# Optimization experiments

Measured on AMD Instinct MI355X. Metric: run time of the kernel, lower is better.

Reference implementation:

```python
import jax, jax.numpy as jnp
import numpy as np

GROUPS = 32
EPS = 1e-6


def setup_inputs() -> dict:
    key = jax.random.key(0)
    ks = jax.random.split(key, 8)
    B, H, W, D, C = 4, 16, 16, 16, 512
    s = 1.0 / np.sqrt(C)  # lecun-normal-ish scale for dense kernels
    return {
        "x": jax.random.normal(ks[0], (B, H, W, D, C), dtype=jnp.float32),
        "gn_scale": jnp.ones((C,), jnp.float32),
        "gn_bias": jnp.zeros((C,), jnp.float32),
        "wq": jax.random.normal(ks[1], (C, C), jnp.float32) * s,
        "bq": jnp.zeros((C,), jnp.float32),
        "wk": jax.random.normal(ks[2], (C, C), jnp.float32) * s,
        "bk": jnp.zeros((C,), jnp.float32),
        "wv": jax.random.normal(ks[3], (C, C), jnp.float32) * s,
        "bv": jnp.zeros((C,), jnp.float32),
        "wp": jax.random.normal(ks[4], (C, C), jnp.float32) * s,
        "bp": jnp.zeros((C,), jnp.float32),
    }


def _group_norm(x, scale, bias):
    B, H, W, D, C = x.shape
    xg = x.reshape(B, H, W, D, GROUPS, C // GROUPS)
    mean = xg.mean(axis=(1, 2, 3, 5), keepdims=True)
    var = xg.var(axis=(1, 2, 3, 5), keepdims=True)
    xn = (xg - mean) * jax.lax.rsqrt(var + EPS)
    return xn.reshape(B, H, W, D, C) * scale + bias


def reference(x, gn_scale, gn_bias, wq, bq, wk, bk, wv, bv, wp, bp):
    B, H, W, D, C = x.shape
    h = _group_norm(x, gn_scale, gn_bias)
    hf = h.reshape(B, H * W * D, C)  # flatten spatial (attention axes 1,2,3)
    q = hf @ wq + bq
    k = hf @ wk + bk
    v = hf @ wv + bv
    # full dot-product attention over flattened (H,W,D) tokens, single head
    q = q * (C ** -0.5)
    logits = jnp.einsum("bqc,bkc->bqk", q, k)  # [B, N, N]
    attn = jax.nn.softmax(logits, axis=-1)
    o = jnp.einsum("bqk,bkc->bqc", attn, v)
    o = o @ wp + bp
    return x + o.reshape(B, H, W, D, C)
```

## Files before the change

### kernel.cpp

```cpp
#include <hip/hip_runtime.h>
#include <stdint.h>

typedef __bf16  bf16x8 __attribute__((ext_vector_type(8)));
typedef short   s16x8  __attribute__((ext_vector_type(8)));
typedef float   f32x4  __attribute__((ext_vector_type(4)));

__device__ inline short f2bf(float f) {
  union { float f; uint32_t u; } v; v.f = f;
  uint32_t r = v.u + 0x7FFFu + ((v.u >> 16) & 1u);
  return (short)(r >> 16);
}


__global__ __launch_bounds__(256) void gn_stats_k(const float* __restrict__ x,
                                                  float* __restrict__ mean,
                                                  float* __restrict__ rstd) {
  int bg = blockIdx.x;
  int b = bg >> 5, g = bg & 31;
  int tid = threadIdx.x;
  const float* base = x + (size_t)b * 4096 * 512 + g * 16;
  float s = 0.f, q = 0.f;
  for (int i = tid; i < 16384; i += 256) {
    int n = i >> 2, sub = i & 3;
    float4 v = *(const float4*)(base + (size_t)n * 512 + sub * 4);
    s += v.x + v.y + v.z + v.w;
    q += v.x * v.x + v.y * v.y + v.z * v.z + v.w * v.w;
  }
  for (int off = 32; off > 0; off >>= 1) {
    s += __shfl_down(s, off, 64);
    q += __shfl_down(q, off, 64);
  }
  __shared__ float rs[4], rq[4];
  int w = tid >> 6;
  if ((tid & 63) == 0) { rs[w] = s; rq[w] = q; }
  __syncthreads();
  if (tid == 0) {
    float S = rs[0] + rs[1] + rs[2] + rs[3];
    float Q = rq[0] + rq[1] + rq[2] + rq[3];
    float m = S * (1.f / 65536.f);
    float var = Q * (1.f / 65536.f) - m * m;
    mean[bg] = m;
    rstd[bg] = rsqrtf(var + 1e-6f);
  }
}

__global__ __launch_bounds__(256) void gn_apply_k(const float* __restrict__ x,
                                                  const float* __restrict__ mean,
                                                  const float* __restrict__ rstd,
                                                  const float* __restrict__ sc,
                                                  const float* __restrict__ bi,
                                                  short* __restrict__ h) {
  size_t i4 = ((size_t)blockIdx.x * 256 + threadIdx.x) * 4;
  int c = (int)(i4 & 511);
  int tok = (int)(i4 >> 9);
  int b = tok >> 12;
  int bg = b * 32 + (c >> 4);
  float m = mean[bg], r = rstd[bg];
  float4 v = *(const float4*)(x + i4);
  float4 s = *(const float4*)(sc + c);
  float4 bb = *(const float4*)(bi + c);
  short4 o;
  o.x = f2bf((v.x - m) * r * s.x + bb.x);
  o.y = f2bf((v.y - m) * r * s.y + bb.y);
  o.z = f2bf((v.z - m) * r * s.z + bb.z);
  o.w = f2bf((v.w - m) * r * s.w + bb.w);
  *(short4*)(h + i4) = o;
}

__global__ __launch_bounds__(256) void wconv_k(const float* __restrict__ wq,
                                               const float* __restrict__ wk,
                                               const float* __restrict__ wv,
                                               const float* __restrict__ wp,
                                               short* __restrict__ wt) {
  int i = blockIdx.x * 256 + threadIdx.x;
  int widx = i >> 18, rem = i & 262143;
  int c = rem >> 9, j = rem & 511;
  const float* w = widx == 0 ? wq : widx == 1 ? wk : widx == 2 ? wv : wp;
  wt[(size_t)widx * 262144 + (size_t)j * 512 + c] = f2bf(w[(size_t)c * 512 + j]);
}

__global__ __launch_bounds__(256) void gemm_k(const short* __restrict__ A,
                                              const short* __restrict__ Bt,
                                              const float* __restrict__ bias,
                                              const float* __restrict__ xres,
                                              short* __restrict__ outb,
                                              float* __restrict__ outf, int mode) {
  __shared__ __attribute__((aligned(16))) short As[128 * 32];
  __shared__ __attribute__((aligned(16))) short Bs[128 * 32];
  int tid = threadIdx.x;
  int w = tid >> 6, lane = tid & 63, quad = lane >> 4, mrow = lane & 15;
  int wm = w >> 1, wn = w & 1;
  int m0 = blockIdx.x * 128, n0 = blockIdx.y * 128;

  const f32x4 fz = {0.f, 0.f, 0.f, 0.f};
  f32x4 acc[4][4];
#pragma unroll
  for (int i = 0; i < 4; i++)
#pragma unroll
    for (int j = 0; j < 4; j++) acc[i][j] = fz;

  int srow = tid >> 2;
  int scol = (tid & 3) * 8;

  for (int k0 = 0; k0 < 512; k0 += 32) {
    __syncthreads();
#pragma unroll
    for (int i = 0; i < 2; i++) {
      const short* ga = A + (size_t)(m0 + i * 64 + srow) * 512 + k0 + scol;
      const short* gb = Bt + (size_t)(n0 + i * 64 + srow) * 512 + k0 + scol;
      char* la = (char*)As + i * 4096 + w * 1024;
      char* lb = (char*)Bs + i * 4096 + w * 1024;
      __builtin_amdgcn_global_load_lds((__attribute__((address_space(1))) void*)ga,
                                       (__attribute__((address_space(3))) void*)la, 16, 0, 0);
      __builtin_amdgcn_global_load_lds((__attribute__((address_space(1))) void*)gb,
                                       (__attribute__((address_space(3))) void*)lb, 16, 0, 0);
    }
    __syncthreads();
    bf16x8 af[4], bfv[4];
#pragma unroll
    for (int mi = 0; mi < 4; mi++)
      af[mi] = *(const bf16x8*)&As[(wm * 64 + mi * 16 + mrow) * 32 + quad * 8];
#pragma unroll
    for (int ni = 0; ni < 4; ni++)
      bfv[ni] = *(const bf16x8*)&Bs[(wn * 64 + ni * 16 + mrow) * 32 + quad * 8];
#pragma unroll
    for (int mi = 0; mi < 4; mi++)
#pragma unroll
      for (int ni = 0; ni < 4; ni++)
        acc[mi][ni] = __builtin_amdgcn_mfma_f32_16x16x32_bf16(af[mi], bfv[ni], acc[mi][ni], 0, 0, 0);
  }

#pragma unroll
  for (int mi = 0; mi < 4; mi++)
#pragma unroll
    for (int ni = 0; ni < 4; ni++) {
      int col = n0 + wn * 64 + ni * 16 + mrow;
      float bv = bias[col];
#pragma unroll
      for (int r = 0; r < 4; r++) {
        int row = m0 + wm * 64 + mi * 16 + quad * 4 + r;
        float val = acc[mi][ni][r] + bv;
        if (mode == 0) {
          outb[(size_t)row * 512 + col] = f2bf(val);
        } else if (mode == 1) {
          int b = row >> 12, t = row & 4095;
          outb[(size_t)b * (512 * 4096) + (size_t)col * 4096 + t] = f2bf(val);
        } else {
          size_t idx = (size_t)row * 512 + col;
          outf[idx] = xres[idx] + val;
        }
      }
    }
}

__global__ __launch_bounds__(256, 1) void flash_k(const short* __restrict__ Q,
                                                  const short* __restrict__ K,
                                                  const short* __restrict__ Vt,
                                                  short* __restrict__ O) {
  __shared__ __attribute__((aligned(16))) short Ks[2][16384];
  int L = blockIdx.x;
  int b = (L & 7) >> 1;
  int q0 = (((L >> 3) << 1) | (L & 1)) * 64;
  int tid = threadIdx.x;
  int w = tid >> 6, lane = tid & 63, quad = lane >> 4, m = lane & 15;
  const size_t batch_off = (size_t)b * 4096 * 512;
  const float scale2 = 0.06375872f;

  bf16x8 qf[16];
#pragma unroll
  for (int s = 0; s < 16; s++)
    qf[s] = *(const bf16x8*)&Q[batch_off + (size_t)(q0 + w * 16 + m) * 512 + s * 32 + quad * 8];

  const f32x4 fz = {0.f, 0.f, 0.f, 0.f};
  f32x4 oacc[32];
#pragma unroll
  for (int i = 0; i < 32; i++) oacc[i] = fz;
  float mrun = -1e30f, lrun = 0.f;

#pragma unroll
  for (int i = 0; i < 8; i++) {
    int ksb = w * 16 + i * 2;
    const short* gk = K + batch_off + (size_t)(lane & 31) * 512 + (size_t)(ksb + (lane >> 5)) * 8;
    __builtin_amdgcn_global_load_lds((__attribute__((address_space(1))) void*)gk,
                                     (__attribute__((address_space(3))) void*)&Ks[0][ksb * 256],
                                     16, 0, 0);
  }

  for (int it = 0; it < 128; ++it) {
    int t0 = it * 32;
    int buf = it & 1;
    __syncthreads();
    if (it < 127) {
      int t1 = t0 + 32;
#pragma unroll
      for (int i = 0; i < 8; i++) {
        int ksb = w * 16 + i * 2;
        const short* gk = K + batch_off + (size_t)(t1 + (lane & 31)) * 512 +
                          (size_t)(ksb + (lane >> 5)) * 8;
        __builtin_amdgcn_global_load_lds((__attribute__((address_space(1))) void*)gk,
                                         (__attribute__((address_space(3))) void*)&Ks[buf ^ 1][ksb * 256],
                                         16, 0, 0);
      }
    }
    bf16x8 vf[32];
#pragma unroll
    for (int ct = 0; ct < 32; ct++)
      vf[ct] = *(const bf16x8*)&Vt[batch_off + (size_t)(ct * 16 + m) * 4096 + t0 + quad * 8];
    f32x4 s0a = fz, s0b = fz, s1a = fz, s1b = fz;
#pragma unroll
    for (int s = 0; s < 16; s++) {
      bf16x8 k0 = *(const bf16x8*)&Ks[buf][((s * 4 + quad) * 32 + m) * 8];
      bf16x8 k1 = *(const bf16x8*)&Ks[buf][((s * 4 + quad) * 32 + 16 + m) * 8];
      if (s & 1) {
        s0b = __builtin_amdgcn_mfma_f32_16x16x32_bf16(k0, qf[s], s0b, 0, 0, 0);
        s1b = __builtin_amdgcn_mfma_f32_16x16x32_bf16(k1, qf[s], s1b, 0, 0, 0);
      } else {
        s0a = __builtin_amdgcn_mfma_f32_16x16x32_bf16(k0, qf[s], s0a, 0, 0, 0);
        s1a = __builtin_amdgcn_mfma_f32_16x16x32_bf16(k1, qf[s], s1a, 0, 0, 0);
      }
    }
    float v0[4], v1[4];
    float mx = -1e30f;
#pragma unroll
    for (int r = 0; r < 4; r++) {
      v0[r] = (s0a[r] + s0b[r]) * scale2;
      v1[r] = (s1a[r] + s1b[r]) * scale2;
      mx = fmaxf(mx, fmaxf(v0[r], v1[r]));
    }
    mx = fmaxf(mx, __shfl_xor(mx, 16, 64));
    mx = fmaxf(mx, __shfl_xor(mx, 32, 64));
    float mn = fmaxf(mrun, mx);
    float alpha = exp2f(mrun - mn);
    mrun = mn;
    float p0[4], p1[4];
    float sum = 0.f;
#pragma unroll
    for (int r = 0; r < 4; r++) {
      p0[r] = exp2f(v0[r] - mn);
      p1[r] = exp2f(v1[r] - mn);
      sum += p0[r] + p1[r];
    }
    sum += __shfl_xor(sum, 16, 64);
    sum += __shfl_xor(sum, 32, 64);
    lrun = lrun * alpha + sum;
    if (__any(alpha != 1.0f)) {
      float al[4];
#pragma unroll
      for (int r = 0; r < 4; r++) al[r] = __shfl(alpha, quad * 4 + r, 64);
#pragma unroll
      for (int i = 0; i < 32; i++)
#pragma unroll
        for (int r = 0; r < 4; r++) oacc[i][r] *= al[r];
    }
    s16x8 pfs;
#pragma unroll
    for (int j = 0; j < 8; j++) {
      int src = ((((quad & 1) * 2 + (j >> 2)) << 4) | m);
      float a0 = __shfl(p0[j & 3], src, 64);
      float a1 = __shfl(p1[j & 3], src, 64);
      pfs[j] = f2bf(quad < 2 ? a0 : a1);
    }
    bf16x8 pf = __builtin_bit_cast(bf16x8, pfs);
#pragma unroll
    for (int ct = 0; ct < 32; ct++)
      oacc[ct] = __builtin_amdgcn_mfma_f32_16x16x32_bf16(pf, vf[ct], oacc[ct], 0, 0, 0);
  }
  float invl = 1.f / lrun;
  float inv[4];
#pragma unroll
  for (int r = 0; r < 4; r++) inv[r] = __shfl(invl, quad * 4 + r, 64);
#pragma unroll
  for (int ct = 0; ct < 32; ct++)
#pragma unroll
    for (int r = 0; r < 4; r++) {
      int row = q0 + w * 16 + quad * 4 + r;
      int col = ct * 16 + m;
      O[batch_off + (size_t)row * 512 + col] = f2bf(oacc[ct][r] * inv[r]);
    }
}

extern "C" void kernel_launch(void* const* d_in, const int* in_sizes, int n_in,
                              void* d_out, int out_size, void* d_ws, size_t ws_size,
                              hipStream_t stream) {
  const float* x  = (const float*)d_in[0];
  const float* gs = (const float*)d_in[1];
  const float* gb = (const float*)d_in[2];
  const float* wq = (const float*)d_in[3];
  const float* bq = (const float*)d_in[4];
  const float* wk = (const float*)d_in[5];
  const float* bk = (const float*)d_in[6];
  const float* wv = (const float*)d_in[7];
  const float* bv = (const float*)d_in[8];
  const float* wp = (const float*)d_in[9];
  const float* bp = (const float*)d_in[10];
  float* out = (float*)d_out;

  char* ws = (char*)d_ws;
  float* mean = (float*)ws;
  float* rstd = (float*)(ws + 512);
  short* h    = (short*)(ws + 1024);
  short* wt   = (short*)(ws + 1024 + 16777216);
  short* Vt   = (short*)(ws + 1024 + 16777216 + 2097152);
  short* Qb   = (short*)d_out;
  short* Kb   = Qb + 8388608;
  short* Ob   = h;

  gn_stats_k<<<128, 256, 0, stream>>>(x, mean, rstd);
  gn_apply_k<<<8192, 256, 0, stream>>>(x, mean, rstd, gs, gb, h);
  wconv_k<<<4096, 256, 0, stream>>>(wq, wk, wv, wp, wt);
  dim3 gg(128, 4);
  gemm_k<<<gg, 256, 0, stream>>>(h, wt,          bq, nullptr, Qb, nullptr, 0);
  gemm_k<<<gg, 256, 0, stream>>>(h, wt + 262144, bk, nullptr, Kb, nullptr, 0);
  gemm_k<<<gg, 256, 0, stream>>>(h, wt + 524288, bv, nullptr, Vt, nullptr, 1);
  flash_k<<<256, 256, 0, stream>>>(Qb, Kb, Vt, Ob);
  gemm_k<<<gg, 256, 0, stream>>>(Ob, wt + 786432, bp, x, nullptr, out, 2);
}
```

Measured before the change: 848.6 us.

## Split flash attention keys across waves and drop LDS K staging

Each block now handles 32 query rows instead of 64, and its four waves split as two query tiles by two halves of the key sequence. The two halves are merged at the end through shared memory using a split-softmax combine. The grid doubles to 512 blocks, with launch bounds raised to allow two blocks per CU. K is now read directly from global memory instead of through double-buffered LDS, and V is loaded per MFMA rather than prefetched into registers. The aim is more parallelism and occupancy, at the cost of less K reuse within a block, more global and cache traffic, and an extra merge step.

```diff
diff --git a/kernel.cpp b/kernel.cpp
--- a/kernel.cpp
+++ b/kernel.cpp
@@ -153,23 +153,26 @@
     }
 }
 
-__global__ __launch_bounds__(256, 1) void flash_k(const short* __restrict__ Q,
+__global__ __launch_bounds__(256, 2) void flash_k(const short* __restrict__ Q,
                                                   const short* __restrict__ K,
                                                   const short* __restrict__ Vt,
                                                   short* __restrict__ O) {
-  __shared__ __attribute__((aligned(16))) short Ks[2][16384];
+  __shared__ float Oz[2][16][512];
+  __shared__ float mS[2][2][16], lS[2][2][16];
   int L = blockIdx.x;
   int b = (L & 7) >> 1;
-  int q0 = (((L >> 3) << 1) | (L & 1)) * 64;
+  int q0 = (((L >> 3) << 1) | (L & 1)) * 32;
   int tid = threadIdx.x;
   int w = tid >> 6, lane = tid & 63, quad = lane >> 4, m = lane & 15;
+  int qt = w & 1, kc = w >> 1;
   const size_t batch_off = (size_t)b * 4096 * 512;
   const float scale2 = 0.06375872f;
 
+  const short* Qrow = Q + batch_off + (size_t)(q0 + qt * 16 + m) * 512;
   bf16x8 qf[16];
 #pragma unroll
   for (int s = 0; s < 16; s++)
-    qf[s] = *(const bf16x8*)&Q[batch_off + (size_t)(q0 + w * 16 + m) * 512 + s * 32 + quad * 8];
+    qf[s] = *(const bf16x8*)&Qrow[s * 32 + quad * 8];
 
   const f32x4 fz = {0.f, 0.f, 0.f, 0.f};
   f32x4 oacc[32];
@@ -177,40 +180,17 @@
   for (int i = 0; i < 32; i++) oacc[i] = fz;
   float mrun = -1e30f, lrun = 0.f;
 
-#pragma unroll
-  for (int i = 0; i < 8; i++) {
-    int ksb = w * 16 + i * 2;
-    const short* gk = K + batch_off + (size_t)(lane & 31) * 512 + (size_t)(ksb + (lane >> 5)) * 8;
-    __builtin_amdgcn_global_load_lds((__attribute__((address_space(1))) void*)gk,
-                                     (__attribute__((address_space(3))) void*)&Ks[0][ksb * 256],
-                                     16, 0, 0);
-  }
-
-  for (int it = 0; it < 128; ++it) {
-    int t0 = it * 32;
-    int buf = it & 1;
-    __syncthreads();
-    if (it < 127) {
-      int t1 = t0 + 32;
-#pragma unroll
-      for (int i = 0; i < 8; i++) {
-        int ksb = w * 16 + i * 2;
-        const short* gk = K + batch_off + (size_t)(t1 + (lane & 31)) * 512 +
-                          (size_t)(ksb + (lane >> 5)) * 8;
-        __builtin_amdgcn_global_load_lds((__attribute__((address_space(1))) void*)gk,
-                                         (__attribute__((address_space(3))) void*)&Ks[buf ^ 1][ksb * 256],
-                                         16, 0, 0);
-      }
-    }
-    bf16x8 vf[32];
-#pragma unroll
-    for (int ct = 0; ct < 32; ct++)
-      vf[ct] = *(const bf16x8*)&Vt[batch_off + (size_t)(ct * 16 + m) * 4096 + t0 + quad * 8];
+  const int tbase = kc * 2048;
+#pragma unroll 1
+  for (int it = 0; it < 64; ++it) {
+    int t0 = tbase + it * 32;
     f32x4 s0a = fz, s0b = fz, s1a = fz, s1b = fz;
+    const short* Kr0 = K + batch_off + (size_t)(t0 + m) * 512;
+    const short* Kr1 = K + batch_off + (size_t)(t0 + 16 + m) * 512;
 #pragma unroll
     for (int s = 0; s < 16; s++) {
-      bf16x8 k0 = *(const bf16x8*)&Ks[buf][((s * 4 + quad) * 32 + m) * 8];
-      bf16x8 k1 = *(const bf16x8*)&Ks[buf][((s * 4 + quad) * 32 + 16 + m) * 8];
+      bf16x8 k0 = *(const bf16x8*)&Kr0[s * 32 + quad * 8];
+      bf16x8 k1 = *(const bf16x8*)&Kr1[s * 32 + quad * 8];
       if (s & 1) {
         s0b = __builtin_amdgcn_mfma_f32_16x16x32_bf16(k0, qf[s], s0b, 0, 0, 0);
         s1b = __builtin_amdgcn_mfma_f32_16x16x32_bf16(k1, qf[s], s1b, 0, 0, 0);
@@ -261,22 +241,46 @@
       pfs[j] = f2bf(quad < 2 ? a0 : a1);
     }
     bf16x8 pf = __builtin_bit_cast(bf16x8, pfs);
+    const short* Vr = Vt + batch_off + (size_t)m * 4096 + t0 + quad * 8;
+#pragma unroll
+    for (int ct = 0; ct < 32; ct++) {
+      bf16x8 vf = *(const bf16x8*)&Vr[(size_t)ct * 16 * 4096];
+      oacc[ct] = __builtin_amdgcn_mfma_f32_16x16x32_bf16(pf, vf, oacc[ct], 0, 0, 0);
+    }
+  }
+  if (lane < 16) { mS[qt][kc][lane] = mrun; lS[qt][kc][lane] = lrun; }
+  __syncthreads();
+  float mo = mS[qt][kc ^ 1][m];
+  float mt = fmaxf(mrun, mo);
+  float f  = exp2f(mrun - mt);
+  float fr[4];
+#pragma unroll
+  for (int r = 0; r < 4; r++) fr[r] = __shfl(f, quad * 4 + r, 64);
+  if (kc == 1) {
 #pragma unroll
     for (int ct = 0; ct < 32; ct++)
-      oacc[ct] = __builtin_amdgcn_mfma_f32_16x16x32_bf16(pf, vf[ct], oacc[ct], 0, 0, 0);
-  }
-  float invl = 1.f / lrun;
-  float inv[4];
-#pragma unroll
-  for (int r = 0; r < 4; r++) inv[r] = __shfl(invl, quad * 4 + r, 64);
-#pragma unroll
-  for (int ct = 0; ct < 32; ct++)
-#pragma unroll
-    for (int r = 0; r < 4; r++) {
-      int row = q0 + w * 16 + quad * 4 + r;
-      int col = ct * 16 + m;
-      O[batch_off + (size_t)row * 512 + col] = f2bf(oacc[ct][r] * inv[r]);
-    }
+#pragma unroll
+      for (int r = 0; r < 4; r++)
+        Oz[qt][quad * 4 + r][ct * 16 + m] = oacc[ct][r] * fr[r];
+  }
+  __syncthreads();
+  if (kc == 0) {
+    float m1 = mS[qt][1][m], l1 = lS[qt][1][m];
+    float ltot = lrun * f + l1 * exp2f(m1 - mt);
+    float invl = 1.f / ltot;
+    float ir[4];
+#pragma unroll
+    for (int r = 0; r < 4; r++) ir[r] = __shfl(invl, quad * 4 + r, 64);
+#pragma unroll
+    for (int ct = 0; ct < 32; ct++)
+#pragma unroll
+      for (int r = 0; r < 4; r++) {
+        float val = oacc[ct][r] * fr[r] + Oz[qt][quad * 4 + r][ct * 16 + m];
+        int row = q0 + qt * 16 + quad * 4 + r;
+        int col = ct * 16 + m;
+        O[batch_off + (size_t)row * 512 + col] = f2bf(val * ir[r]);
+      }
+  }
 }
 
 extern "C" void kernel_launch(void* const* d_in, const int* in_sizes, int n_in,
@@ -312,6 +316,6 @@
   gemm_k<<<gg, 256, 0, stream>>>(h, wt,          bq, nullptr, Qb, nullptr, 0);
   gemm_k<<<gg, 256, 0, stream>>>(h, wt + 262144, bk, nullptr, Kb, nullptr, 0);
   gemm_k<<<gg, 256, 0, stream>>>(h, wt + 524288, bv, nullptr, Vt, nullptr, 1);
-  flash_k<<<256, 256, 0, stream>>>(Qb, Kb, Vt, Ob);
+  flash_k<<<512, 256, 0, stream>>>(Qb, Kb, Vt, Ob);
   gemm_k<<<gg, 256, 0, stream>>>(Ob, wt + 786432, bp, x, nullptr, out, 2);
 }
```

Result: slower. 1.135 ms (+33.8%).

## Split flash attention waves across output channels with smaller query tiles

Applied to the files above, without the earlier changes.

The flash kernel now gives each block 16 query rows instead of 64. Its four waves split the 512 output channels (128 each) rather than the query rows, and the grid grows from 256 to 1024 blocks with a two-blocks-per-CU launch bound. This cuts the output accumulator registers fourfold and prefetches the next V tile into registers one iteration ahead. The P fragments are also packed to bf16 before the shuffle, halving the shuffle count. In exchange, every wave recomputes the same QK^T scores, and K is streamed into LDS four times as often overall.

```diff
diff --git a/kernel.cpp b/kernel.cpp
--- a/kernel.cpp
+++ b/kernel.cpp
@@ -10,6 +10,7 @@
   uint32_t r = v.u + 0x7FFFu + ((v.u >> 16) & 1u);
   return (short)(r >> 16);
 }
+__device__ inline uint32_t f2bf_u(float f) { return (uint32_t)(uint16_t)f2bf(f); }
 
 
 __global__ __launch_bounds__(256) void gn_stats_k(const float* __restrict__ x,
@@ -153,28 +154,30 @@
     }
 }
 
-__global__ __launch_bounds__(256, 1) void flash_k(const short* __restrict__ Q,
+__global__ __launch_bounds__(256, 2) void flash_k(const short* __restrict__ Q,
                                                   const short* __restrict__ K,
                                                   const short* __restrict__ Vt,
                                                   short* __restrict__ O) {
   __shared__ __attribute__((aligned(16))) short Ks[2][16384];
   int L = blockIdx.x;
   int b = (L & 7) >> 1;
-  int q0 = (((L >> 3) << 1) | (L & 1)) * 64;
+  int qt = ((L >> 3) << 1) | (L & 1);
+  int q0 = qt * 16;
   int tid = threadIdx.x;
   int w = tid >> 6, lane = tid & 63, quad = lane >> 4, m = lane & 15;
   const size_t batch_off = (size_t)b * 4096 * 512;
   const float scale2 = 0.06375872f;
 
+  const short* Qrow = Q + batch_off + (size_t)(q0 + m) * 512;
   bf16x8 qf[16];
 #pragma unroll
   for (int s = 0; s < 16; s++)
-    qf[s] = *(const bf16x8*)&Q[batch_off + (size_t)(q0 + w * 16 + m) * 512 + s * 32 + quad * 8];
+    qf[s] = *(const bf16x8*)&Qrow[s * 32 + quad * 8];
 
   const f32x4 fz = {0.f, 0.f, 0.f, 0.f};
-  f32x4 oacc[32];
-#pragma unroll
-  for (int i = 0; i < 32; i++) oacc[i] = fz;
+  f32x4 oacc[8];
+#pragma unroll
+  for (int i = 0; i < 8; i++) oacc[i] = fz;
   float mrun = -1e30f, lrun = 0.f;
 
 #pragma unroll
@@ -186,6 +189,13 @@
                                      16, 0, 0);
   }
 
+  const short* Vbase = Vt + batch_off + (size_t)(w * 128 + m) * 4096 + quad * 8;
+  bf16x8 vc[8];
+#pragma unroll
+  for (int ct = 0; ct < 8; ct++)
+    vc[ct] = *(const bf16x8*)&Vbase[(size_t)ct * 16 * 4096];
+
+#pragma unroll 1
   for (int it = 0; it < 128; ++it) {
     int t0 = it * 32;
     int buf = it & 1;
@@ -202,10 +212,13 @@
                                          16, 0, 0);
       }
     }
-    bf16x8 vf[32];
-#pragma unroll
-    for (int ct = 0; ct < 32; ct++)
-      vf[ct] = *(const bf16x8*)&Vt[batch_off + (size_t)(ct * 16 + m) * 4096 + t0 + quad * 8];
+    bf16x8 vn[8];
+    if (it < 127) {
+      int t1 = t0 + 32;
+#pragma unroll
+      for (int ct = 0; ct < 8; ct++)
+        vn[ct] = *(const bf16x8*)&Vbase[(size_t)ct * 16 * 4096 + t1];
+    }
     f32x4 s0a = fz, s0b = fz, s1a = fz, s1b = fz;
 #pragma unroll
     for (int s = 0; s < 16; s++) {
@@ -248,34 +261,41 @@
 #pragma unroll
       for (int r = 0; r < 4; r++) al[r] = __shfl(alpha, quad * 4 + r, 64);
 #pragma unroll
-      for (int i = 0; i < 32; i++)
+      for (int i = 0; i < 8; i++)
 #pragma unroll
         for (int r = 0; r < 4; r++) oacc[i][r] *= al[r];
     }
+    uint32_t pk[4];
+#pragma unroll
+    for (int r = 0; r < 4; r++)
+      pk[r] = f2bf_u(p0[r]) | (f2bf_u(p1[r]) << 16);
     s16x8 pfs;
 #pragma unroll
     for (int j = 0; j < 8; j++) {
       int src = ((((quad & 1) * 2 + (j >> 2)) << 4) | m);
-      float a0 = __shfl(p0[j & 3], src, 64);
-      float a1 = __shfl(p1[j & 3], src, 64);
-      pfs[j] = f2bf(quad < 2 ? a0 : a1);
+      uint32_t pv = (uint32_t)__shfl((int)pk[j & 3], src, 64);
+      pfs[j] = (short)(quad < 2 ? (pv & 0xffffu) : (pv >> 16));
     }
     bf16x8 pf = __builtin_bit_cast(bf16x8, pfs);
 #pragma unroll
-    for (int ct = 0; ct < 32; ct++)
-      oacc[ct] = __builtin_amdgcn_mfma_f32_16x16x32_bf16(pf, vf[ct], oacc[ct], 0, 0, 0);
+    for (int ct = 0; ct < 8; ct++)
+      oacc[ct] = __builtin_amdgcn_mfma_f32_16x16x32_bf16(pf, vc[ct], oacc[ct], 0, 0, 0);
+    if (it < 127) {
+#pragma unroll
+      for (int ct = 0; ct < 8; ct++) vc[ct] = vn[ct];
+    }
   }
   float invl = 1.f / lrun;
-  float inv[4];
-#pragma unroll
-  for (int r = 0; r < 4; r++) inv[r] = __shfl(invl, quad * 4 + r, 64);
-#pragma unroll
-  for (int ct = 0; ct < 32; ct++)
+  float ir[4];
+#pragma unroll
+  for (int r = 0; r < 4; r++) ir[r] = __shfl(invl, quad * 4 + r, 64);
+#pragma unroll
+  for (int ct = 0; ct < 8; ct++)
 #pragma unroll
     for (int r = 0; r < 4; r++) {
-      int row = q0 + w * 16 + quad * 4 + r;
-      int col = ct * 16 + m;
-      O[batch_off + (size_t)row * 512 + col] = f2bf(oacc[ct][r] * inv[r]);
+      int row = q0 + quad * 4 + r;
+      int col = w * 128 + ct * 16 + m;
+      O[batch_off + (size_t)row * 512 + col] = f2bf(oacc[ct][r] * ir[r]);
     }
 }
 
@@ -312,6 +332,6 @@
   gemm_k<<<gg, 256, 0, stream>>>(h, wt,          bq, nullptr, Qb, nullptr, 0);
   gemm_k<<<gg, 256, 0, stream>>>(h, wt + 262144, bk, nullptr, Kb, nullptr, 0);
   gemm_k<<<gg, 256, 0, stream>>>(h, wt + 524288, bv, nullptr, Vt, nullptr, 1);
-  flash_k<<<256, 256, 0, stream>>>(Qb, Kb, Vt, Ob);
+  flash_k<<<1024, 256, 0, stream>>>(Qb, Kb, Vt, Ob);
   gemm_k<<<gg, 256, 0, stream>>>(Ob, wt + 786432, bp, x, nullptr, out, 2);
 }
```

Result: slower. 1.300 ms (+53.2%).

## Stage V tiles through double-buffered LDS and pack P bf16 before shuffling

Applied to the files above, without the earlier changes.

Each block now loads the V^T tile for the next key step into a second double-buffered LDS array with async global_load_lds, alongside K. Previously every wave read all 32 V fragments straight from global memory on each iteration. The P fragment is converted to bf16 and two values are packed per 32-bit register before the cross-lane shuffle, which halves the shuffle count. LDS use doubles to 128KB and the occupancy hint in launch_bounds is dropped, which may limit residency to one block per CU.

```diff
diff --git a/kernel.cpp b/kernel.cpp
--- a/kernel.cpp
+++ b/kernel.cpp
@@ -10,6 +10,7 @@
   uint32_t r = v.u + 0x7FFFu + ((v.u >> 16) & 1u);
   return (short)(r >> 16);
 }
+__device__ inline uint32_t f2bf_u(float f) { return (uint32_t)(uint16_t)f2bf(f); }
 
 
 __global__ __launch_bounds__(256) void gn_stats_k(const float* __restrict__ x,
@@ -153,11 +154,12 @@
     }
 }
 
-__global__ __launch_bounds__(256, 1) void flash_k(const short* __restrict__ Q,
-                                                  const short* __restrict__ K,
-                                                  const short* __restrict__ Vt,
-                                                  short* __restrict__ O) {
+__global__ __launch_bounds__(256) void flash_k(const short* __restrict__ Q,
+                                               const short* __restrict__ K,
+                                               const short* __restrict__ Vt,
+                                               short* __restrict__ O) {
   __shared__ __attribute__((aligned(16))) short Ks[2][16384];
+  __shared__ __attribute__((aligned(16))) short Vs[2][16384];
   int L = blockIdx.x;
   int b = (L & 7) >> 1;
   int q0 = (((L >> 3) << 1) | (L & 1)) * 64;
@@ -166,10 +168,11 @@
   const size_t batch_off = (size_t)b * 4096 * 512;
   const float scale2 = 0.06375872f;
 
+  const short* Qrow = Q + batch_off + (size_t)(q0 + w * 16 + m) * 512;
   bf16x8 qf[16];
 #pragma unroll
   for (int s = 0; s < 16; s++)
-    qf[s] = *(const bf16x8*)&Q[batch_off + (size_t)(q0 + w * 16 + m) * 512 + s * 32 + quad * 8];
+    qf[s] = *(const bf16x8*)&Qrow[s * 32 + quad * 8];
 
   const f32x4 fz = {0.f, 0.f, 0.f, 0.f};
   f32x4 oacc[32];
@@ -185,7 +188,16 @@
                                      (__attribute__((address_space(3))) void*)&Ks[0][ksb * 256],
                                      16, 0, 0);
   }
-
+#pragma unroll
+  for (int i = 0; i < 8; i++) {
+    int ct = w * 8 + i;
+    const short* gv = Vt + batch_off + (size_t)(ct * 16 + m) * 4096 + quad * 8;
+    __builtin_amdgcn_global_load_lds((__attribute__((address_space(1))) void*)gv,
+                                     (__attribute__((address_space(3))) void*)&Vs[0][ct * 512],
+                                     16, 0, 0);
+  }
+
+#pragma unroll 1
   for (int it = 0; it < 128; ++it) {
     int t0 = it * 32;
     int buf = it & 1;
@@ -201,11 +213,15 @@
                                          (__attribute__((address_space(3))) void*)&Ks[buf ^ 1][ksb * 256],
                                          16, 0, 0);
       }
-    }
-    bf16x8 vf[32];
-#pragma unroll
-    for (int ct = 0; ct < 32; ct++)
-      vf[ct] = *(const bf16x8*)&Vt[batch_off + (size_t)(ct * 16 + m) * 4096 + t0 + quad * 8];
+#pragma unroll
+      for (int i = 0; i < 8; i++) {
+        int ct = w * 8 + i;
+        const short* gv = Vt + batch_off + (size_t)(ct * 16 + m) * 4096 + t1 + quad * 8;
+        __builtin_amdgcn_global_load_lds((__attribute__((address_space(1))) void*)gv,
+                                         (__attribute__((address_space(3))) void*)&Vs[buf ^ 1][ct * 512],
+                                         16, 0, 0);
+      }
+    }
     f32x4 s0a = fz, s0b = fz, s1a = fz, s1b = fz;
 #pragma unroll
     for (int s = 0; s < 16; s++) {
@@ -252,30 +268,35 @@
 #pragma unroll
         for (int r = 0; r < 4; r++) oacc[i][r] *= al[r];
     }
+    uint32_t pk[4];
+#pragma unroll
+    for (int r = 0; r < 4; r++)
+      pk[r] = f2bf_u(p0[r]) | (f2bf_u(p1[r]) << 16);
     s16x8 pfs;
 #pragma unroll
     for (int j = 0; j < 8; j++) {
       int src = ((((quad & 1) * 2 + (j >> 2)) << 4) | m);
-      float a0 = __shfl(p0[j & 3], src, 64);
-      float a1 = __shfl(p1[j & 3], src, 64);
-      pfs[j] = f2bf(quad < 2 ? a0 : a1);
+      uint32_t pv = (uint32_t)__shfl((int)pk[j & 3], src, 64);
+      pfs[j] = (short)(quad < 2 ? (pv & 0xffffu) : (pv >> 16));
     }
     bf16x8 pf = __builtin_bit_cast(bf16x8, pfs);
 #pragma unroll
-    for (int ct = 0; ct < 32; ct++)
-      oacc[ct] = __builtin_amdgcn_mfma_f32_16x16x32_bf16(pf, vf[ct], oacc[ct], 0, 0, 0);
+    for (int ct = 0; ct < 32; ct++) {
+      bf16x8 vf = *(const bf16x8*)&Vs[buf][(ct * 64 + lane) * 8];
+      oacc[ct] = __builtin_amdgcn_mfma_f32_16x16x32_bf16(pf, vf, oacc[ct], 0, 0, 0);
+    }
   }
   float invl = 1.f / lrun;
-  float inv[4];
-#pragma unroll
-  for (int r = 0; r < 4; r++) inv[r] = __shfl(invl, quad * 4 + r, 64);
+  float ir[4];
+#pragma unroll
+  for (int r = 0; r < 4; r++) ir[r] = __shfl(invl, quad * 4 + r, 64);
 #pragma unroll
   for (int ct = 0; ct < 32; ct++)
 #pragma unroll
     for (int r = 0; r < 4; r++) {
       int row = q0 + w * 16 + quad * 4 + r;
       int col = ct * 16 + m;
-      O[batch_off + (size_t)row * 512 + col] = f2bf(oacc[ct][r] * inv[r]);
+      O[batch_off + (size_t)row * 512 + col] = f2bf(oacc[ct][r] * ir[r]);
     }
 }
 
```

Measured after the change: 768.6 us. -9.4%, faster.
